# Kernel tuning notes

Measured on AMD Instinct MI355X. Metric: run time of the kernel, lower is better.

Reference implementation:

```python
import math
import jax, jax.numpy as jnp
import numpy as np

B, CIN, COUT, K, Z, H, W = 8, 512, 512, 3, 512, 64, 64


def setup_inputs() -> dict:
    key = jax.random.key(0)
    k1, k2, k3, k4 = jax.random.split(key, 4)
    inp = {
        "input": jax.random.normal(k1, (B, CIN, H, W), dtype=jnp.float32),
        "style": jax.random.normal(k2, (B, Z), dtype=jnp.float32),
        # base conv weight: [1, out, in, k, k]
        "weight": jax.random.normal(k3, (1, COUT, CIN, K, K), dtype=jnp.float32),
        # EqualLinear modulation params (lr_mul=1, bias_init=1)
        "mod_w": jax.random.normal(k4, (CIN, Z), dtype=jnp.float32),
        "mod_b": jnp.ones((CIN,), dtype=jnp.float32),
    }
    return inp


def reference(input, style, weight, mod_w, mod_b):
    # EqualLinear: scale = 1/sqrt(z_dim), lr_mul = 1, no activation
    z_dim = mod_w.shape[1]
    mod_scale = 1.0 / math.sqrt(z_dim)
    s = style @ (mod_w * mod_scale).T + mod_b  # [B, in]

    # modulated per-sample weights: scale * base_weight * style
    in_ch, k = weight.shape[2], weight.shape[-1]
    conv_scale = 1.0 / math.sqrt(in_ch * k * k)
    w = conv_scale * weight * s[:, None, :, None, None]  # [B, out, in, k, k]

    pad = k // 2

    def conv_one(x, wb):  # x: [in, H, W], wb: [out, in, k, k]
        return jax.lax.conv_general_dilated(
            x[None], wb, window_strides=(1, 1),
            padding=[(pad, pad), (pad, pad)],
            dimension_numbers=("NCHW", "OIHW", "NCHW"),
        )[0]

    out = jax.vmap(conv_one)(input, w)  # [B, out, H, W]
    return out
```

## Files before the change

### kernel.cpp

```cpp
#include <hip/hip_runtime.h>
#include <hip/hip_bf16.h>

#define BB   8
#define CIN  512
#define COUT 512
#define ZD   512
#define HH   64
#define WW   64

#define MOD_SCALE  0.04419417382415922f
#define CONV_SCALE 0.014731391274719742f

typedef __bf16 bf16x8 __attribute__((ext_vector_type(8)));
typedef float  f32x4  __attribute__((ext_vector_type(4)));
typedef float  f32x16 __attribute__((ext_vector_type(16)));

static __device__ __forceinline__ unsigned short f32_to_bf16_rne(float f) {
    unsigned int u = __float_as_uint(f);
    u = (u + 0x7FFFu + ((u >> 16) & 1u)) >> 16;
    return (unsigned short)u;
}

__global__ void k_style(const float* __restrict__ style, const float* __restrict__ mod_w,
                        const float* __restrict__ mod_b, float* __restrict__ sconv) {
    int wid  = blockIdx.x * 4 + (threadIdx.x >> 6);
    int lane = threadIdx.x & 63;
    int b = wid >> 9;
    int i = wid & 511;
    const float4* st = (const float4*)(style + (size_t)b * ZD);
    const float4* mw = (const float4*)(mod_w + (size_t)i * ZD);
    float4 a0 = st[lane],      b0 = mw[lane];
    float4 a1 = st[lane + 64], b1 = mw[lane + 64];
    float sum = a0.x*b0.x + a0.y*b0.y + a0.z*b0.z + a0.w*b0.w
              + a1.x*b1.x + a1.y*b1.y + a1.z*b1.z + a1.w*b1.w;
    #pragma unroll
    for (int off = 32; off > 0; off >>= 1) sum += __shfl_down(sum, off);
    if (lane == 0) sconv[wid] = (sum * MOD_SCALE + mod_b[i]) * CONV_SCALE;
}

__global__ void k_zero_border(unsigned short* __restrict__ xs2p) {
    int b = blockIdx.y;
    int p = blockIdx.x * 4 + (threadIdx.x >> 6);
    int lane = threadIdx.x & 63;
    int h, w;
    if (p < 66)       { h = 0;       w = p; }
    else if (p < 132) { h = 65;      w = p - 66; }
    else if (p < 196) { h = p - 131; w = 0; }
    else              { h = p - 195; w = 65; }
    int4 z = {0, 0, 0, 0};
    *(int4*)&xs2p[((size_t)(b * 66 + h) * 66 + w) * 512 + lane * 8] = z;
}

__global__ void k_scale_input(const float* __restrict__ input, const float* __restrict__ sconv,
                              unsigned short* __restrict__ xs2p) {
    int i0 = blockIdx.x * 32;
    int h  = blockIdx.y;
    int b  = blockIdx.z;
    __shared__ unsigned short lds[64][40];
    #pragma unroll
    for (int r = 0; r < 8; ++r) {
        int ii = r * 4 + (threadIdx.x >> 6);
        int w  = threadIdx.x & 63;
        float v = input[(((size_t)b * CIN + i0 + ii) * HH + h) * WW + w];
        float s = sconv[b * CIN + i0 + ii];
        lds[w][ii] = f32_to_bf16_rne(v * s);
    }
    __syncthreads();
    int w = threadIdx.x >> 2, q = threadIdx.x & 3;
    int4 val = *(const int4*)&lds[w][q * 8];
    *(int4*)&xs2p[((size_t)(b * 66 + h + 1) * 66 + (w + 1)) * 512 + i0 + q * 8] = val;
}

__global__ void k_weight(const float* __restrict__ weight, unsigned short* __restrict__ w3) {
    int t = blockIdx.x * 256 + threadIdx.x;
    int o = t >> 9, i = t & 511;
    int c = i >> 5, g = (i >> 3) & 3, il = i & 7;
    int h = o >> 8, ol = o & 255;
    const float* src = weight + ((size_t)o * CIN + i) * 9;
    #pragma unroll
    for (int p = 0; p < 9; ++p) {
        size_t gran = ((size_t)(c * 9 + p) * 2 + h) * 1024 + g * 256 + ol;
        w3[gran * 8 + il] = f32_to_bf16_rne(src[p]);
    }
}

#define GLD(srcp, ldsbyte)                                                        \
    __builtin_amdgcn_global_load_lds(                                             \
        (const __attribute__((address_space(1))) unsigned int*)(srcp),            \
        (__attribute__((address_space(3))) unsigned int*)(smb + (ldsbyte)),       \
        16, 0, 0)

#define TAP(t, DOX, DOW, ENDCH, C, N) {                                           \
    if (DOW) {                                                                    \
        aW##N[0][0] = *(const bf16x8*)(pA);                                       \
        aW##N[1][0] = *(const bf16x8*)(pA + 512);                                 \
        aW##N[0][1] = *(const bf16x8*)(pA + 8192);                                \
        aW##N[1][1] = *(const bf16x8*)(pA + 8704);                                \
        pA += 32768;                                                              \
    }                                                                             \
    if ((DOX) && (t) == 0) { GLD(sxn +  0, xwr + 0 * 8192 + wdst);                \
                             GLD(sxn + 16, xwr + 1 * 8192 + wdst); }              \
    if ((DOX) && (t) == 1) { GLD(sxn + 32, xwr + 2 * 8192 + wdst);                \
                             GLD(sxn + 48, xwr + 3 * 8192 + wdst); }              \
    {   const int kh_ = (t) / 3, kw_ = (t) % 3;                                   \
        const char* xb = smb + xrd + boff + (kh_ * 66 + kw_) * 16;                \
        bfr[0][0] = *(const bf16x8*)(xb);                                         \
        bfr[1][0] = *(const bf16x8*)(xb + 512);                                   \
        bfr[2][0] = *(const bf16x8*)(xb + 1056);                                  \
        bfr[3][0] = *(const bf16x8*)(xb + 1568);                                  \
        bfr[0][1] = *(const bf16x8*)(xb + 16384);                                 \
        bfr[1][1] = *(const bf16x8*)(xb + 16896);                                 \
        bfr[2][1] = *(const bf16x8*)(xb + 17440);                                 \
        bfr[3][1] = *(const bf16x8*)(xb + 17952);                                 \
    }                                                                             \
    __builtin_amdgcn_s_setprio(1);                                                \
    _Pragma("unroll") for (int h = 0; h < 2; ++h)                                 \
      _Pragma("unroll") for (int mt = 0; mt < 2; ++mt)                            \
        _Pragma("unroll") for (int nt = 0; nt < 4; ++nt)                          \
            acc[mt][nt] = __builtin_amdgcn_mfma_f32_32x32x16_bf16(                \
                aW##C[mt][h], bfr[nt][h], acc[mt][nt], 0, 0, 0);                  \
    __builtin_amdgcn_s_setprio(0);                                                \
    if (ENDCH) { asm volatile("s_waitcnt vmcnt(4)" ::: "memory");                 \
                 __builtin_amdgcn_s_barrier(); xrd ^= 32768; sxn += 64; }         \
}

#define CHUNKE_FULL {                                                             \
    const int xwr = xrd ^ 32768;                                                  \
    TAP(0, 1, 1, 0, E, O) TAP(1, 1, 1, 0, O, E) TAP(2, 0, 1, 0, E, O)             \
    TAP(3, 0, 1, 0, O, E) TAP(4, 0, 1, 0, E, O) TAP(5, 0, 1, 0, O, E)             \
    TAP(6, 0, 1, 0, E, O) TAP(7, 0, 1, 0, O, E) TAP(8, 0, 1, 1, E, O) }
#define CHUNKO_FULL {                                                             \
    const int xwr = xrd ^ 32768;                                                  \
    TAP(0, 1, 1, 0, O, E) TAP(1, 1, 1, 0, E, O) TAP(2, 0, 1, 0, O, E)             \
    TAP(3, 0, 1, 0, E, O) TAP(4, 0, 1, 0, O, E) TAP(5, 0, 1, 0, E, O)             \
    TAP(6, 0, 1, 0, O, E) TAP(7, 0, 1, 0, E, O) TAP(8, 0, 1, 1, O, E) }
#define CHUNKO_TAIL {                                                             \
    const int xwr = 0; (void)xwr;                                                 \
    TAP(0, 0, 1, 0, O, E) TAP(1, 0, 1, 0, E, O) TAP(2, 0, 1, 0, O, E)             \
    TAP(3, 0, 1, 0, E, O) TAP(4, 0, 1, 0, O, E) TAP(5, 0, 1, 0, E, O)             \
    TAP(6, 0, 1, 0, O, E) TAP(7, 0, 1, 0, E, O) TAP(8, 0, 0, 0, O, E) }

__global__ __launch_bounds__(512, 2)
void k_conv(const unsigned short* __restrict__ xs2p, const unsigned short* __restrict__ w3,
            float* __restrict__ out) {
    __shared__ unsigned short smem[32768];
    char* smb = (char*)smem;

    const int tid  = threadIdx.x;
    const int wid  = tid >> 6, lane = tid & 63;
    const int wm4  = wid >> 1, wr2  = wid & 1;
    const int l31  = lane & 31, l5  = lane >> 5;
    const int half = blockIdx.x;
    const int oc0  = half * 256;
    const int y0   = blockIdx.y * 4;
    const int b    = blockIdx.z;

    const int p_lin = wid * 64 + lane;
    const int xrow  = p_lin / 66;
    const int xcol  = p_lin - xrow * 66;
    const char* srcX = (const char*)xs2p;
    if (p_lin < 396)
        srcX += ((size_t)(b * 66 + y0 + xrow) * 66 + xcol) * 1024;

    const char* pA = (const char*)w3 + (size_t)half * 16384
                   + ((size_t)(l5 * 256 + wm4 * 64 + l31)) * 16;
    const int wdst = p_lin * 16;

    GLD(srcX +  0, 0 * 8192 + wdst);
    GLD(srcX + 16, 1 * 8192 + wdst);
    GLD(srcX + 32, 2 * 8192 + wdst);
    GLD(srcX + 48, 3 * 8192 + wdst);
    bf16x8 aWE[2][2], aWO[2][2], bfr[4][2];
    aWE[0][0] = *(const bf16x8*)(pA);
    aWE[1][0] = *(const bf16x8*)(pA + 512);
    aWE[0][1] = *(const bf16x8*)(pA + 8192);
    aWE[1][1] = *(const bf16x8*)(pA + 8704);
    pA += 32768;
    asm volatile("s_waitcnt vmcnt(4)" ::: "memory");
    __builtin_amdgcn_s_barrier();

    f32x16 acc[2][4];
    #pragma unroll
    for (int mt = 0; mt < 2; ++mt)
        #pragma unroll
        for (int nt = 0; nt < 4; ++nt)
            acc[mt][nt] = (f32x16)(0.f);

    const int boff = l5 * 8192 + (wr2 * 2 * 66 + l31) * 16;

    int xrd = 0;
    const char* sxn = srcX + 64;

    for (int c2 = 0; c2 < 7; ++c2) {
        CHUNKE_FULL
        CHUNKO_FULL
    }
    CHUNKE_FULL
    CHUNKO_TAIL

    #pragma unroll
    for (int mt = 0; mt < 2; ++mt)
        #pragma unroll
        for (int nt = 0; nt < 4; ++nt) {
            const int y  = y0 + wr2 * 2 + (nt >> 1);
            const int px = (nt & 1) * 32 + l31;
            #pragma unroll
            for (int r = 0; r < 16; ++r) {
                int row = (r & 3) + 8 * (r >> 2) + 4 * l5;
                int oc  = oc0 + wm4 * 64 + mt * 32 + row;
                out[((size_t)(b * COUT + oc) << 12) + y * 64 + px] = acc[mt][nt][r];
            }
        }
}

extern "C" void kernel_launch(void* const* d_in, const int* in_sizes, int n_in,
                              void* d_out, int out_size, void* d_ws, size_t ws_size,
                              hipStream_t stream) {
    const float* input  = (const float*)d_in[0];
    const float* style  = (const float*)d_in[1];
    const float* weight = (const float*)d_in[2];
    const float* mod_w  = (const float*)d_in[3];
    const float* mod_b  = (const float*)d_in[4];
    float* out = (float*)d_out;

    const size_t xs2p_bytes = (size_t)BB * 66 * 66 * 512 * 2;
    const size_t w3_bytes   = (size_t)144 * 2 * 1024 * 8 * 2;
    const size_t need = 16384 + xs2p_bytes + w3_bytes;
    if (ws_size < need) return;

    float*          sconv = (float*)d_ws;
    unsigned short* xs2p  = (unsigned short*)((char*)d_ws + 16384);
    unsigned short* w3    = (unsigned short*)((char*)d_ws + 16384 + xs2p_bytes);

    hipLaunchKernelGGL(k_style,       dim3(1024),      dim3(256), 0, stream, style, mod_w, mod_b, sconv);
    hipLaunchKernelGGL(k_weight,      dim3(1024),      dim3(256), 0, stream, weight, w3);
    hipLaunchKernelGGL(k_zero_border, dim3(65, 8),     dim3(256), 0, stream, xs2p);
    hipLaunchKernelGGL(k_scale_input, dim3(16, 64, 8), dim3(256), 0, stream, input, sconv, xs2p);
    hipLaunchKernelGGL(k_conv,        dim3(2, 16, 8),  dim3(512), 0, stream, xs2p, w3, out);
}
```

Baseline: 167.2 us.

## Split conv blocks into 256-thread, 128-output-channel tiles with reworked input staging

```diff
diff --git a/kernel.cpp b/kernel.cpp
--- a/kernel.cpp
+++ b/kernel.cpp
@@ -98,10 +98,10 @@
         aW##N[1][1] = *(const bf16x8*)(pA + 8704);                                \
         pA += 32768;                                                              \
     }                                                                             \
-    if ((DOX) && (t) == 0) { GLD(sxn +  0, xwr + 0 * 8192 + wdst);                \
-                             GLD(sxn + 16, xwr + 1 * 8192 + wdst); }              \
-    if ((DOX) && (t) == 1) { GLD(sxn + 32, xwr + 2 * 8192 + wdst);                \
-                             GLD(sxn + 48, xwr + 3 * 8192 + wdst); }              \
+    if ((DOX) && (t) < 4) {                                                       \
+        GLD(sx0 + (t) * 16, xwr + (t) * 8192 + wdst0);                            \
+        GLD(sx1 + (t) * 16, xwr + (t) * 8192 + wdst1);                            \
+    }                                                                             \
     {   const int kh_ = (t) / 3, kw_ = (t) % 3;                                   \
         const char* xb = smb + xrd + boff + (kh_ * 66 + kw_) * 16;                \
         bfr[0][0] = *(const bf16x8*)(xb);                                         \
@@ -120,19 +120,20 @@
             acc[mt][nt] = __builtin_amdgcn_mfma_f32_32x32x16_bf16(                \
                 aW##C[mt][h], bfr[nt][h], acc[mt][nt], 0, 0, 0);                  \
     __builtin_amdgcn_s_setprio(0);                                                \
-    if (ENDCH) { asm volatile("s_waitcnt vmcnt(4)" ::: "memory");                 \
-                 __builtin_amdgcn_s_barrier(); xrd ^= 32768; sxn += 64; }         \
+    if (ENDCH) { asm volatile("s_waitcnt vmcnt(0)" ::: "memory");                 \
+                 __builtin_amdgcn_s_barrier();                                    \
+                 xrd ^= 32768; sx0 += 64; sx1 += 64; }                            \
 }
 
 #define CHUNKE_FULL {                                                             \
     const int xwr = xrd ^ 32768;                                                  \
-    TAP(0, 1, 1, 0, E, O) TAP(1, 1, 1, 0, O, E) TAP(2, 0, 1, 0, E, O)             \
-    TAP(3, 0, 1, 0, O, E) TAP(4, 0, 1, 0, E, O) TAP(5, 0, 1, 0, O, E)             \
+    TAP(0, 1, 1, 0, E, O) TAP(1, 1, 1, 0, O, E) TAP(2, 1, 1, 0, E, O)             \
+    TAP(3, 1, 1, 0, O, E) TAP(4, 0, 1, 0, E, O) TAP(5, 0, 1, 0, O, E)             \
     TAP(6, 0, 1, 0, E, O) TAP(7, 0, 1, 0, O, E) TAP(8, 0, 1, 1, E, O) }
 #define CHUNKO_FULL {                                                             \
     const int xwr = xrd ^ 32768;                                                  \
-    TAP(0, 1, 1, 0, O, E) TAP(1, 1, 1, 0, E, O) TAP(2, 0, 1, 0, O, E)             \
-    TAP(3, 0, 1, 0, E, O) TAP(4, 0, 1, 0, O, E) TAP(5, 0, 1, 0, E, O)             \
+    TAP(0, 1, 1, 0, O, E) TAP(1, 1, 1, 0, E, O) TAP(2, 1, 1, 0, O, E)             \
+    TAP(3, 1, 1, 0, E, O) TAP(4, 0, 1, 0, O, E) TAP(5, 0, 1, 0, E, O)             \
     TAP(6, 0, 1, 0, O, E) TAP(7, 0, 1, 0, E, O) TAP(8, 0, 1, 1, O, E) }
 #define CHUNKO_TAIL {                                                             \
     const int xwr = 0; (void)xwr;                                                 \
@@ -140,7 +141,7 @@
     TAP(3, 0, 1, 0, E, O) TAP(4, 0, 1, 0, O, E) TAP(5, 0, 1, 0, E, O)             \
     TAP(6, 0, 1, 0, O, E) TAP(7, 0, 1, 0, E, O) TAP(8, 0, 0, 0, O, E) }
 
-__global__ __launch_bounds__(512, 2)
+__global__ __launch_bounds__(256, 2)
 void k_conv(const unsigned short* __restrict__ xs2p, const unsigned short* __restrict__ w3,
             float* __restrict__ out) {
     __shared__ unsigned short smem[32768];
@@ -150,33 +151,39 @@
     const int wid  = tid >> 6, lane = tid & 63;
     const int wm4  = wid >> 1, wr2  = wid & 1;
     const int l31  = lane & 31, l5  = lane >> 5;
-    const int half = blockIdx.x;
-    const int oc0  = half * 256;
-    const int y0   = blockIdx.y * 4;
+    const int y0   = blockIdx.x * 4;
+    const int ocq  = blockIdx.y;
     const int b    = blockIdx.z;
 
-    const int p_lin = wid * 64 + lane;
-    const int xrow  = p_lin / 66;
-    const int xcol  = p_lin - xrow * 66;
-    const char* srcX = (const char*)xs2p;
-    if (p_lin < 396)
-        srcX += ((size_t)(b * 66 + y0 + xrow) * 66 + xcol) * 1024;
-
-    const char* pA = (const char*)w3 + (size_t)half * 16384
-                   + ((size_t)(l5 * 256 + wm4 * 64 + l31)) * 16;
-    const int wdst = p_lin * 16;
-
-    GLD(srcX +  0, 0 * 8192 + wdst);
-    GLD(srcX + 16, 1 * 8192 + wdst);
-    GLD(srcX + 32, 2 * 8192 + wdst);
-    GLD(srcX + 48, 3 * 8192 + wdst);
+    const char* sx0 = (const char*)xs2p;
+    const char* sx1 = (const char*)xs2p;
+    {
+        int p0 = tid,      r0 = p0 / 66, c0 = p0 - r0 * 66;
+        int p1 = tid + 256;
+        sx0 += ((size_t)(b * 66 + y0 + r0) * 66 + c0) * 1024;
+        if (p1 < 396) {
+            int r1 = p1 / 66, c1 = p1 - r1 * 66;
+            sx1 += ((size_t)(b * 66 + y0 + r1) * 66 + c1) * 1024;
+        }
+    }
+    const int wdst0 = tid * 16;
+    const int wdst1 = (tid + 256) * 16;
+
+    const char* pA = (const char*)w3 + (size_t)(ocq >> 1) * 16384
+                   + ((size_t)(l5 * 256 + (ocq & 1) * 128 + wm4 * 64 + l31)) * 16;
+
+    GLD(sx0 +  0, 0 * 8192 + wdst0); GLD(sx1 +  0, 0 * 8192 + wdst1);
+    GLD(sx0 + 16, 1 * 8192 + wdst0); GLD(sx1 + 16, 1 * 8192 + wdst1);
+    GLD(sx0 + 32, 2 * 8192 + wdst0); GLD(sx1 + 32, 2 * 8192 + wdst1);
+    GLD(sx0 + 48, 3 * 8192 + wdst0); GLD(sx1 + 48, 3 * 8192 + wdst1);
+    sx0 += 64; sx1 += 64;
     bf16x8 aWE[2][2], aWO[2][2], bfr[4][2];
     aWE[0][0] = *(const bf16x8*)(pA);
     aWE[1][0] = *(const bf16x8*)(pA + 512);
     aWE[0][1] = *(const bf16x8*)(pA + 8192);
     aWE[1][1] = *(const bf16x8*)(pA + 8704);
     pA += 32768;
-    asm volatile("s_waitcnt vmcnt(4)" ::: "memory");
+    asm volatile("s_waitcnt vmcnt(0)" ::: "memory");
     __builtin_amdgcn_s_barrier();
 
     f32x16 acc[2][4];
@@ -189,7 +196,6 @@
     const int boff = l5 * 8192 + (wr2 * 2 * 66 + l31) * 16;
 
     int xrd = 0;
-    const char* sxn = srcX + 64;
 
     for (int c2 = 0; c2 < 7; ++c2) {
         CHUNKE_FULL
@@ -207,7 +213,7 @@
             #pragma unroll
             for (int r = 0; r < 16; ++r) {
                 int row = (r & 3) + 8 * (r >> 2) + 4 * l5;
-                int oc  = oc0 + wm4 * 64 + mt * 32 + row;
+                int oc  = ocq * 128 + wm4 * 64 + mt * 32 + row;
                 out[((size_t)(b * COUT + oc) << 12) + y * 64 + px] = acc[mt][nt][r];
             }
         }
@@ -236,5 +242,5 @@
     hipLaunchKernelGGL(k_weight,      dim3(1024),      dim3(256), 0, stream, weight, w3);
     hipLaunchKernelGGL(k_zero_border, dim3(65, 8),     dim3(256), 0, stream, xs2p);
     hipLaunchKernelGGL(k_scale_input, dim3(16, 64, 8), dim3(256), 0, stream, input, sconv, xs2p);
-    hipLaunchKernelGGL(k_conv,        dim3(2, 16, 8),  dim3(512), 0, stream, xs2p, w3, out);
-}
+    hipLaunchKernelGGL(k_conv,        dim3(16, 4, 8),  dim3(256), 0, stream, xs2p, w3, out);
+}
```

Result: slower. 181.8 us (+8.7%).
